# Optimization experiments

Measured on AMD Instinct MI355X. Metric: run time of the kernel, lower is better.

The kernel has to match this reference:

```python
import jax, jax.numpy as jnp
import numpy as np

LPC_ORDER = 32
GAMMA = 1.0  # get_gamma(1, None) == 1


def setup_inputs() -> dict:
    key = jax.random.key(0)
    # PARCOR coefficients, magnitude < 1 for stability; shape (..., M+1)
    k = jax.random.uniform(key, (16, 65536, LPC_ORDER + 1), dtype=jnp.float32)
    return {"k": k}


def reference(k):
    # Levinson-style PARCOR -> LPC recursion (diffsptk par2lpc).
    # a starts as k / gamma; for m = 2..M: a[1:m] += k[m] * flip(a[1:m])
    M1 = k.shape[-1]
    a = k / GAMMA
    for m in range(2, M1):  # fixed, small unrolled loop over order
        km = k[..., m : m + 1]          # (..., 1)  reflection coefficient
        am = a[..., 1:m]                 # (..., m-1) current LPC prefix
        a = a.at[..., 1:m].set(am + km * am[..., ::-1])
    return a
```

## Files before the change

kernel.cpp:

```cpp
#include <hip/hip_runtime.h>

#define M1   33
#define BLK  128
#define BLK_ELEMS (BLK * M1)
#define BLK_VEC4  (BLK_ELEMS / 4)
#define VEC_FULL  (BLK_VEC4 / BLK)
#define VEC_REM   (BLK_VEC4 - VEC_FULL * BLK)

__global__ __launch_bounds__(BLK)
void parcor_to_lpc_kernel(const float* __restrict__ k, float* __restrict__ out) {
    __shared__ float lds[BLK_ELEMS];

    const size_t base = (size_t)blockIdx.x * BLK_ELEMS;
    const float4* __restrict__ gsrc4 = (const float4*)(k + base);
    float4* __restrict__ gdst4 = (float4*)(out + base);
    float4* lds4 = (float4*)lds;

    #pragma unroll
    for (int i = 0; i < VEC_FULL; ++i)
        lds4[i * BLK + threadIdx.x] = gsrc4[i * BLK + threadIdx.x];
    if (threadIdx.x < VEC_REM)
        lds4[VEC_FULL * BLK + threadIdx.x] = gsrc4[VEC_FULL * BLK + threadIdx.x];
    __syncthreads();

    const int t = threadIdx.x;
    float a[M1];
    #pragma unroll
    for (int j = 0; j < M1; ++j)
        a[j] = lds[t * M1 + j];

    #pragma unroll
    for (int m = 2; m < M1; ++m) {
        const float km = a[m];
        #pragma unroll
        for (int j = 1; 2 * j < m; ++j) {
            const float x = a[j];
            const float y = a[m - j];
            a[j]     = fmaf(km, y, x);
            a[m - j] = fmaf(km, x, y);
        }
        if ((m & 1) == 0) {
            const int j = m >> 1;
            a[j] = fmaf(km, a[j], a[j]);
        }
    }

    #pragma unroll
    for (int j = 0; j < M1; ++j)
        lds[t * M1 + j] = a[j];
    __syncthreads();

    #pragma unroll
    for (int i = 0; i < VEC_FULL; ++i)
        gdst4[i * BLK + threadIdx.x] = lds4[i * BLK + threadIdx.x];
    if (threadIdx.x < VEC_REM)
        gdst4[VEC_FULL * BLK + threadIdx.x] = lds4[VEC_FULL * BLK + threadIdx.x];
}

__global__ void parcor_to_lpc_tail_kernel(const float* __restrict__ k,
                                          float* __restrict__ out,
                                          int row_start, int nrows) {
    const int row = row_start + blockIdx.x * blockDim.x + threadIdx.x;
    if (row >= nrows) return;
    const float* src = k + (size_t)row * M1;
    float* dst = out + (size_t)row * M1;
    float a[M1];
    #pragma unroll
    for (int j = 0; j < M1; ++j) a[j] = src[j];
    #pragma unroll
    for (int m = 2; m < M1; ++m) {
        const float km = a[m];
        #pragma unroll
        for (int j = 1; 2 * j < m; ++j) {
            const float x = a[j];
            const float y = a[m - j];
            a[j]     = fmaf(km, y, x);
            a[m - j] = fmaf(km, x, y);
        }
        if ((m & 1) == 0) {
            const int j = m >> 1;
            a[j] = fmaf(km, a[j], a[j]);
        }
    }
    #pragma unroll
    for (int j = 0; j < M1; ++j) dst[j] = a[j];
}

extern "C" void kernel_launch(void* const* d_in, const int* in_sizes, int n_in,
                              void* d_out, int out_size, void* d_ws, size_t ws_size,
                              hipStream_t stream) {
    const float* k = (const float*)d_in[0];
    float* out = (float*)d_out;

    const int nrows = in_sizes[0] / M1;
    const int nblk  = nrows / BLK;
    const int rem   = nrows - nblk * BLK;

    if (nblk > 0)
        parcor_to_lpc_kernel<<<nblk, BLK, 0, stream>>>(k, out);
    if (rem > 0)
        parcor_to_lpc_tail_kernel<<<(rem + BLK - 1) / BLK, BLK, 0, stream>>>(
            k, out, nblk * BLK, nrows);
}
```

Baseline: 237.8 us.

## Make kernel persistent with double-buffered async global-to-LDS tile prefetch

Replaces the one-tile-per-block kernel with a persistent kernel of 1024 blocks that loop over tiles. While a tile is computed, the next tile is prefetched into a second LDS buffer with global_load_lds. The current tile's results are held in registers and written out during the next iteration. The goal is to overlap global loads and stores with the recurrence compute. The cost is twice the LDS per block, more registers for the deferred store, and a fixed grid size that may reduce occupancy or latency hiding. The tail kernel's block size also changes.

```diff
diff --git a/kernel.cpp b/kernel.cpp
--- a/kernel.cpp
+++ b/kernel.cpp
@@ -1,60 +1,107 @@
 #include <hip/hip_runtime.h>
 
-#define M1   33
-#define BLK  128
-#define BLK_ELEMS (BLK * M1)
-#define BLK_VEC4  (BLK_ELEMS / 4)
-#define VEC_FULL  (BLK_VEC4 / BLK)
-#define VEC_REM   (BLK_VEC4 - VEC_FULL * BLK)
+#define M1         33
+#define BLK        128
+#define TILE_ELEMS (BLK * M1)
+#define TILE_VEC4  (TILE_ELEMS / 4)
+#define VEC_FULL   (TILE_VEC4 / BLK)
+#define VEC_REM    (TILE_VEC4 - VEC_FULL * BLK)
+#define NBLK       1024
+
+typedef __attribute__((address_space(3))) void  lds_void_t;
+typedef const __attribute__((address_space(1))) void gbl_void_t;
+
+__device__ __forceinline__ void gll16(const float4* gsrc, float4* ldsdst) {
+    __builtin_amdgcn_global_load_lds((gbl_void_t*)gsrc, (lds_void_t*)ldsdst, 16, 0, 0);
+}
+
+__device__ __forceinline__ void prefetch_tile(const float* __restrict__ k,
+                                              float* lbuf, size_t tile, int tid) {
+    const float4* g = (const float4*)(k + tile * TILE_ELEMS);
+    float4* l = (float4*)lbuf;
+    #pragma unroll
+    for (int i = 0; i < VEC_FULL; ++i)
+        gll16(g + i * BLK + tid, l + i * BLK + tid);
+    if (tid < VEC_REM)
+        gll16(g + VEC_FULL * BLK + tid, l + VEC_FULL * BLK + tid);
+}
 
 __global__ __launch_bounds__(BLK)
-void parcor_to_lpc_kernel(const float* __restrict__ k, float* __restrict__ out) {
-    __shared__ float lds[BLK_ELEMS];
+void parcor_persist_kernel(const float* __restrict__ k, float* __restrict__ out,
+                           int ntiles) {
+    __shared__ float buf[2][TILE_ELEMS];
+    const int tid = threadIdx.x;
 
-    const size_t base = (size_t)blockIdx.x * BLK_ELEMS;
-    const float4* __restrict__ gsrc4 = (const float4*)(k + base);
-    float4* __restrict__ gdst4 = (float4*)(out + base);
-    float4* lds4 = (float4*)lds;
+    const int t0 = blockIdx.x;
+    if (t0 < ntiles)
+        prefetch_tile(k, buf[0], (size_t)t0, tid);
 
-    #pragma unroll
-    for (int i = 0; i < VEC_FULL; ++i)
-        lds4[i * BLK + threadIdx.x] = gsrc4[i * BLK + threadIdx.x];
-    if (threadIdx.x < VEC_REM)
-        lds4[VEC_FULL * BLK + threadIdx.x] = gsrc4[VEC_FULL * BLK + threadIdx.x];
-    __syncthreads();
+    float4 st[VEC_FULL];
+    float4 st_rem;
+    float* st_base = nullptr;
 
-    const int t = threadIdx.x;
-    float a[M1];
-    #pragma unroll
-    for (int j = 0; j < M1; ++j)
-        a[j] = lds[t * M1 + j];
+    int parity = 0;
+    for (int t = t0; t < ntiles; t += NBLK, parity ^= 1) {
+        __syncthreads();
 
-    #pragma unroll
-    for (int m = 2; m < M1; ++m) {
-        const float km = a[m];
+        const int tn = t + NBLK;
+        if (tn < ntiles)
+            prefetch_tile(k, buf[parity ^ 1], (size_t)tn, tid);
+
+        if (st_base) {
+            float4* gd = (float4*)st_base;
+            #pragma unroll
+            for (int i = 0; i < VEC_FULL; ++i)
+                gd[i * BLK + tid] = st[i];
+            if (tid < VEC_REM)
+                gd[VEC_FULL * BLK + tid] = st_rem;
+        }
+
+        float* cur = buf[parity];
+        float a[M1];
         #pragma unroll
-        for (int j = 1; 2 * j < m; ++j) {
-            const float x = a[j];
-            const float y = a[m - j];
-            a[j]     = fmaf(km, y, x);
-            a[m - j] = fmaf(km, x, y);
+        for (int j = 0; j < M1; ++j)
+            a[j] = cur[tid * M1 + j];
+
+        #pragma unroll
+        for (int m = 2; m < M1; ++m) {
+            const float km = a[m];
+            #pragma unroll
+            for (int j = 1; 2 * j < m; ++j) {
+                const float x = a[j];
+                const float y = a[m - j];
+                a[j]     = fmaf(km, y, x);
+                a[m - j] = fmaf(km, x, y);
+            }
+            if ((m & 1) == 0) {
+                const int j = m >> 1;
+                a[j] = fmaf(km, a[j], a[j]);
+            }
         }
-        if ((m & 1) == 0) {
-            const int j = m >> 1;
-            a[j] = fmaf(km, a[j], a[j]);
-        }
+
+        #pragma unroll
+        for (int j = 0; j < M1; ++j)
+            cur[tid * M1 + j] = a[j];
+
+        __syncthreads();
+
+        float4* l4 = (float4*)cur;
+        #pragma unroll
+        for (int i = 0; i < VEC_FULL; ++i)
+            st[i] = l4[i * BLK + tid];
+        if (tid < VEC_REM)
+            st_rem = l4[VEC_FULL * BLK + tid];
+        st_base = out + (size_t)t * TILE_ELEMS;
     }
 
-    #pragma unroll
-    for (int j = 0; j < M1; ++j)
-        lds[t * M1 + j] = a[j];
-    __syncthreads();
-
-    #pragma unroll
-    for (int i = 0; i < VEC_FULL; ++i)
-        gdst4[i * BLK + threadIdx.x] = lds4[i * BLK + threadIdx.x];
-    if (threadIdx.x < VEC_REM)
-        gdst4[VEC_FULL * BLK + threadIdx.x] = lds4[VEC_FULL * BLK + threadIdx.x];
+    if (st_base) {
+        float4* gd = (float4*)st_base;
+        #pragma unroll
+        for (int i = 0; i < VEC_FULL; ++i)
+            gd[i * BLK + tid] = st[i];
+        if (tid < VEC_REM)
+            gd[VEC_FULL * BLK + tid] = st_rem;
+    }
 }
 
 __global__ void parcor_to_lpc_tail_kernel(const float* __restrict__ k,
@@ -92,13 +139,15 @@
     const float* k = (const float*)d_in[0];
     float* out = (float*)d_out;
 
-    const int nrows = in_sizes[0] / M1;
-    const int nblk  = nrows / BLK;
-    const int rem   = nrows - nblk * BLK;
+    const int nrows  = in_sizes[0] / M1;
+    const int ntiles = nrows / BLK;
+    const int rem    = nrows - ntiles * BLK;
 
-    if (nblk > 0)
-        parcor_to_lpc_kernel<<<nblk, BLK, 0, stream>>>(k, out);
+    if (ntiles > 0) {
+        const int grid = ntiles < NBLK ? ntiles : NBLK;
+        parcor_persist_kernel<<<grid, BLK, 0, stream>>>(k, out, ntiles);
+    }
     if (rem > 0)
-        parcor_to_lpc_tail_kernel<<<(rem + BLK - 1) / BLK, BLK, 0, stream>>>(
-            k, out, nblk * BLK, nrows);
+        parcor_to_lpc_tail_kernel<<<(rem + 255) / 256, 256, 0, stream>>>(
+            k, out, ntiles * BLK, nrows);
 }
```

New measurement: 253.4 us. +6.6%, slower.
